# Kernel tuning notes

Hardware: AMD Instinct MI355X
Metric: run time of the kernel (lower is better)

## Reference

```python
import jax, jax.numpy as jnp
import numpy as np

EPS = 1e-12

def sage_layer(x, src, dst, Wl, Wr, b, n_nodes):
    # mean aggregation of source-node features into destination nodes
    msgs = x[src]                                            # [E, F] gather
    s = jax.ops.segment_sum(msgs, dst, num_segments=n_nodes)  # [N, F]
    cnt = jax.ops.segment_sum(jnp.ones((src.shape[0],), x.dtype), dst, num_segments=n_nodes)
    agg = s / jnp.maximum(cnt, 1.0)[:, None]                 # mean; 0 for isolated nodes
    out = agg @ Wl + b + x @ Wr                              # lin_l(agg) + lin_r(x_i)
    norm = jnp.linalg.norm(out, axis=-1, keepdims=True)      # normalize=True -> L2 norm
    return out / jnp.maximum(norm, EPS)


def setup_inputs() -> dict:
    key = jax.random.key(0)
    ks = jax.random.split(key, 8)
    N, E, F = 100000, 1200000, 64
    H1, H2, OUT = 64, 32, 10  # hidden_channels//2, hidden_channels//4, output_dim
    x = jax.random.normal(ks[0], (N, F), dtype=jnp.float32)
    edge_index = jax.random.randint(ks[1], (2, E), 0, N, dtype=jnp.int64)
    def glorot(k, fin, fout):
        lim = np.sqrt(6.0 / (fin + fout)).astype(np.float32)
        return jax.random.uniform(k, (fin, fout), jnp.float32, -lim, lim)
    return {
        "x": x,
        "edge_index": edge_index,
        "W1l": glorot(ks[2], F, H1), "W1r": glorot(ks[3], F, H1), "b1": jnp.zeros((H1,), jnp.float32),
        "W2l": glorot(ks[4], H1, H2), "W2r": glorot(ks[5], H1, H2), "b2": jnp.zeros((H2,), jnp.float32),
        "W3l": glorot(ks[6], H2, OUT), "W3r": glorot(ks[7], H2, OUT), "b3": jnp.zeros((OUT,), jnp.float32),
    }


def reference(x, edge_index, W1l, W1r, b1, W2l, W2r, b2, W3l, W3r, b3):
    n = x.shape[0]
    src, dst = edge_index[0], edge_index[1]
    h = jax.nn.relu(sage_layer(x, src, dst, W1l, W1r, b1, n))
    h = jax.nn.relu(sage_layer(h, src, dst, W2l, W2r, b2, n))
    h = sage_layer(h, src, dst, W3l, W3r, b3, n)
    return jax.nn.log_softmax(h, axis=1)
```

## Files before the change

### kernel.cpp

```cpp
#include <hip/hip_runtime.h>
#include <math.h>


typedef __attribute__((ext_vector_type(8))) short short8;
typedef __attribute__((ext_vector_type(4))) float floatx4;
typedef __attribute__((ext_vector_type(2))) float floatx2;

__device__ __forceinline__ unsigned short f2bf(float f) {
    unsigned u = __float_as_uint(f);
    u += 0x7fffu + ((u >> 16) & 1u);
    return (unsigned short)(u >> 16);
}
__device__ __forceinline__ float blo(unsigned u) { return __uint_as_float(u << 16); }
__device__ __forceinline__ float bhi(unsigned u) { return __uint_as_float(u & 0xffff0000u); }
__device__ __forceinline__ unsigned char f2fp8(float f) {
    return (unsigned char)(__builtin_amdgcn_cvt_pk_fp8_f32(f, f, 0, false) & 0xFF);
}


__global__ __launch_bounds__(256) void hist_kernel(
        const int* __restrict__ ei, int* __restrict__ bh, int* __restrict__ sync_ctr,
        int E, int NB, int NBKT) {
    __shared__ int lh[256];
    const int tid = threadIdx.x, blk = blockIdx.x;
    if (blk == 0 && tid == 0) *sync_ctr = 0;
    lh[tid] = 0;
    __syncthreads();
    const int base = blk << 12;
#pragma unroll
    for (int i = 0; i < 16; ++i) {
        const int e = base + (i << 8) + tid;
        if (e < E) atomicAdd(&lh[min((int)(((unsigned)ei[E + e]) >> 9), NBKT - 1)], 1);
    }
    __syncthreads();
    if (tid < NBKT) bh[tid * NB + blk] = lh[tid];
}

__global__ __launch_bounds__(256) void bscan_kernel(
        const int* __restrict__ bh, int* __restrict__ offs, int* __restrict__ btot,
        int* __restrict__ bucket_base, int* __restrict__ sync_ctr,
        int NB, int NBKT) {
    const int lane = threadIdx.x & 63;
    const int w = blockIdx.x * 4 + (threadIdx.x >> 6);
    if (w < NBKT) {
        int running = 0;
        for (int base = 0; base < NB; base += 64) {
            const int j = base + lane;
            const int v = (j < NB) ? bh[w * NB + j] : 0;
            int incl = v;
#pragma unroll
            for (int off = 1; off < 64; off <<= 1) {
                const int t = __shfl_up(incl, off);
                if (lane >= off) incl += t;
            }
            if (j < NB) offs[w * NB + j] = running + incl - v;
            running += __shfl(incl, 63);
        }
        if (lane == 0) btot[w] = running;
    }
    __threadfence();
    __syncthreads();
    __shared__ int amLast;
    if (threadIdx.x == 0) amLast = (atomicAdd(sync_ctr, 1) == (int)gridDim.x - 1);
    __syncthreads();
    if (amLast && threadIdx.x < 64) {
        __threadfence();
        int running = 0;
        for (int base = 0; base < NBKT; base += 64) {
            const int j = base + threadIdx.x;
            const int v = (j < NBKT) ? btot[j] : 0;
            int incl = v;
#pragma unroll
            for (int off = 1; off < 64; off <<= 1) {
                const int t = __shfl_up(incl, off);
                if ((int)threadIdx.x >= off) incl += t;
            }
            if (j < NBKT) bucket_base[j] = running + incl - v;
            running += __shfl(incl, 63);
        }
        if (threadIdx.x == 0) bucket_base[NBKT] = running;
    }
}

__global__ __launch_bounds__(256) void scatter_kernel(
        const int* __restrict__ ei, const int* __restrict__ offs,
        const int* __restrict__ bucket_base, unsigned* __restrict__ ebuf,
        int E, int NB, int NBKT) {
    __shared__ int lcur[256];
    const int tid = threadIdx.x, blk = blockIdx.x;
    if (tid < NBKT) lcur[tid] = bucket_base[tid] + offs[tid * NB + blk];
    __syncthreads();
    const int base = blk << 12;
#pragma unroll
    for (int i = 0; i < 16; ++i) {
        const int e = base + (i << 8) + tid;
        if (e < E) {
            const int s = ei[e];
            const unsigned d = (unsigned)ei[E + e];
            int p = atomicAdd(&lcur[min((int)(d >> 9), NBKT - 1)], 1);
            p = min(p, E - 1);
            ebuf[p] = ((d & 511u) << 17) | (unsigned)s;
        }
    }
}

__global__ __launch_bounds__(512) void bucket_csr_kernel(
        const unsigned* __restrict__ ebuf, const int* __restrict__ bucket_base,
        int* __restrict__ rowptr, int* __restrict__ deg, int* __restrict__ col,
        int N, int E) {
    __shared__ unsigned long long lcnt[512];
    __shared__ int lcur[2048];
    __shared__ int wsum[8];
    const int b = blockIdx.x, tid = threadIdx.x;
    const int q1 = N >> 2, q2 = N >> 1, q3 = (N >> 2) + (N >> 1);
    const int segbase = bucket_base[b];
    const int L = bucket_base[b + 1] - segbase;
    lcnt[tid] = 0ull;
    __syncthreads();
    for (int i = tid; i < L; i += 512) {
        const unsigned p = ebuf[segbase + i];
        const int ln = p >> 17;
        const int s  = (int)(p & 0x1FFFFu);
        const int q  = (s < q2) ? ((s < q1) ? 0 : 1) : ((s < q3) ? 2 : 3);
        atomicAdd(&lcnt[ln], 1ull << (q << 4));
    }
    __syncthreads();
    const unsigned long long cv = lcnt[tid];
    const int f0 = (int)(cv & 0xFFFFu),         f1 = (int)((cv >> 16) & 0xFFFFu);
    const int f2 = (int)((cv >> 32) & 0xFFFFu), f3 = (int)((cv >> 48) & 0xFFFFu);
    const int dnode = f0 + f1 + f2 + f3;
    const int lane = tid & 63, w = tid >> 6;
    int incl = dnode;
#pragma unroll
    for (int off = 1; off < 64; off <<= 1) {
        const int t = __shfl_up(incl, off);
        if (lane >= off) incl += t;
    }
    if (lane == 63) wsum[w] = incl;
    __syncthreads();
    int wbase = 0;
#pragma unroll
    for (int ww = 0; ww < 8; ++ww) if (ww < w) wbase += wsum[ww];
    const int excl = wbase + incl - dnode;
    const int node = (b << 9) + tid;
    if (node < N) { rowptr[node] = segbase + excl; deg[node] = dnode; }
    lcur[tid]        = excl;
    lcur[512 + tid]  = excl + f0;
    lcur[1024 + tid] = excl + f0 + f1;
    lcur[1536 + tid] = excl + f0 + f1 + f2;
    __syncthreads();
    for (int i = tid; i < L; i += 512) {
        const unsigned p = ebuf[segbase + i];
        const int ln = p >> 17;
        const int s  = (int)(p & 0x1FFFFu);
        const int q  = (s < q2) ? ((s < q1) ? 0 : 1) : ((s < q3) ? 2 : 3);
        int pos = atomicAdd(&lcur[(q << 9) + ln], 1);
        pos = min(segbase + pos, E - 1);
        col[pos] = s;
    }
}

template <int K, int F_OUT, int PAD, bool AFP32, bool YL8>
__global__ __launch_bounds__(256) void transform_kernel(
        const void* __restrict__ Ain, const float* __restrict__ Wl,
        const float* __restrict__ Wr, const float* __restrict__ b,
        void* __restrict__ yl, unsigned short* __restrict__ yr, int n) {
    constexpr int KSTEP = K / 32;
    constexpr int NT = PAD / 16;
    const int lane = threadIdx.x & 63;
    const int wid = (blockIdx.x * blockDim.x + threadIdx.x) >> 6;
    const int ntiles = (n + 15) >> 4;
    if (wid >= ntiles) return;
    const int nl = lane & 15, q = lane >> 4;

    short8 Bl[NT][KSTEP], Br[NT][KSTEP];
    float biasv[NT];
#pragma unroll
    for (int t = 0; t < NT; ++t) {
        const int ncol = t * 16 + nl;
        biasv[t] = (ncol < F_OUT) ? b[ncol] : 0.f;
#pragma unroll
        for (int ks = 0; ks < KSTEP; ++ks) {
#pragma unroll
            for (int j = 0; j < 8; ++j) {
                const int k = ks * 32 + q * 8 + j;
                Bl[t][ks][j] = (ncol < F_OUT) ? (short)f2bf(Wl[k * F_OUT + ncol]) : (short)0;
                Br[t][ks][j] = (ncol < F_OUT) ? (short)f2bf(Wr[k * F_OUT + ncol]) : (short)0;
            }
        }
    }

    const int m0 = wid * 16;
    int m = m0 + nl; if (m >= n) m = n - 1;

    short8 a[KSTEP];
#pragma unroll
    for (int ks = 0; ks < KSTEP; ++ks) {
        if (AFP32) {
            const float* p = (const float*)Ain + (size_t)m * K + ks * 32 + q * 8;
#pragma unroll
            for (int j = 0; j < 8; ++j) a[ks][j] = (short)f2bf(p[j]);
        } else {
            union { uint4 u; short8 s; } cvt;
            cvt.u = *(const uint4*)((const unsigned short*)Ain + (size_t)m * K + ks * 32 + q * 8);
            a[ks] = cvt.s;
        }
    }

    floatx4 accl[NT], accr[NT];
#pragma unroll
    for (int t = 0; t < NT; ++t) { accl[t] = {0.f,0.f,0.f,0.f}; accr[t] = {0.f,0.f,0.f,0.f}; }
#pragma unroll
    for (int ks = 0; ks < KSTEP; ++ks) {
#pragma unroll
        for (int t = 0; t < NT; ++t) {
            accl[t] = __builtin_amdgcn_mfma_f32_16x16x32_bf16(a[ks], Bl[t][ks], accl[t], 0, 0, 0);
            accr[t] = __builtin_amdgcn_mfma_f32_16x16x32_bf16(a[ks], Br[t][ks], accr[t], 0, 0, 0);
        }
    }

#pragma unroll
    for (int t = 0; t < NT; ++t) {
        const int ncol = t * 16 + nl;
#pragma unroll
        for (int r = 0; r < 4; ++r) {
            const int node = m0 + q * 4 + r;
            if (node < n) {
                if (YL8)
                    ((unsigned char*)yl)[(size_t)node * PAD + ncol] = f2fp8(accl[t][r]);
                else
                    ((unsigned short*)yl)[(size_t)node * PAD + ncol] = f2bf(accl[t][r]);
                yr[(size_t)node * PAD + ncol] = f2bf(accr[t][r] + biasv[t]);
            }
        }
    }
}

template <int F, int ACT, int PK>
__global__ __launch_bounds__(256) void agg_kernel(
        const void* __restrict__ yl, const unsigned short* __restrict__ yr,
        const int* __restrict__ rowptr, const int* __restrict__ degv,
        const int* __restrict__ col,
        unsigned short* __restrict__ hout, float* __restrict__ fout, int n) {
    constexpr int G = F / 8;
    constexpr int NPW = 64 / G;
    const int lane = threadIdx.x & 63;
    const int wid = (blockIdx.x * blockDim.x + threadIdx.x) >> 6;
    const int g = lane / G, c = lane % G;
    const int node = wid * NPW + g;
    if (node >= n) return;

    const int beg = rowptr[node];
    const int dg  = degv[node];
    const int nmax = n - 1;

    float a0=0.f,a1=0.f,a2=0.f,a3=0.f,a4=0.f,a5=0.f,a6=0.f,a7=0.f;
    int i = 0;
    if (PK == 1) {
        const unsigned char* base = (const unsigned char*)yl + c * 8;
        auto accrow = [&](uint2 t) {
            const floatx2 p0 = __builtin_amdgcn_cvt_pk_f32_fp8((int)t.x, false);
            const floatx2 p1 = __builtin_amdgcn_cvt_pk_f32_fp8((int)t.x, true);
            const floatx2 p2 = __builtin_amdgcn_cvt_pk_f32_fp8((int)t.y, false);
            const floatx2 p3 = __builtin_amdgcn_cvt_pk_f32_fp8((int)t.y, true);
            a0 += p0.x; a1 += p0.y; a2 += p1.x; a3 += p1.y;
            a4 += p2.x; a5 += p2.y; a6 += p3.x; a7 += p3.y;
        };
        if (dg >= 4) {
            int c0 = col[beg], c1 = col[beg+1], c2 = col[beg+2], c3 = col[beg+3];
            for (; i + 8 <= dg; i += 4) {
                const int d0 = col[beg+i+4], d1 = col[beg+i+5];
                const int d2 = col[beg+i+6], d3 = col[beg+i+7];
                const uint2 t0 = *(const uint2*)(base + (size_t)min(c0,nmax) * F);
                const uint2 t1 = *(const uint2*)(base + (size_t)min(c1,nmax) * F);
                const uint2 t2 = *(const uint2*)(base + (size_t)min(c2,nmax) * F);
                const uint2 t3 = *(const uint2*)(base + (size_t)min(c3,nmax) * F);
                accrow(t0); accrow(t1); accrow(t2); accrow(t3);
                c0 = d0; c1 = d1; c2 = d2; c3 = d3;
            }
            const uint2 t0 = *(const uint2*)(base + (size_t)min(c0,nmax) * F);
            const uint2 t1 = *(const uint2*)(base + (size_t)min(c1,nmax) * F);
            const uint2 t2 = *(const uint2*)(base + (size_t)min(c2,nmax) * F);
            const uint2 t3 = *(const uint2*)(base + (size_t)min(c3,nmax) * F);
            accrow(t0); accrow(t1); accrow(t2); accrow(t3);
            i += 4;
        }
        for (; i < dg; ++i)
            accrow(*(const uint2*)(base + (size_t)min(col[beg+i],nmax) * F));
    } else {
        const unsigned short* base = (const unsigned short*)yl + c * 8;
        auto accrow4 = [&](uint4 t) {
            a0 += blo(t.x); a1 += bhi(t.x); a2 += blo(t.y); a3 += bhi(t.y);
            a4 += blo(t.z); a5 += bhi(t.z); a6 += blo(t.w); a7 += bhi(t.w);
        };
        if (dg >= 4) {
            int c0 = col[beg], c1 = col[beg+1], c2 = col[beg+2], c3 = col[beg+3];
            for (; i + 8 <= dg; i += 4) {
                const int d0 = col[beg+i+4], d1 = col[beg+i+5];
                const int d2 = col[beg+i+6], d3 = col[beg+i+7];
                const uint4 t0 = *(const uint4*)(base + (size_t)min(c0,nmax) * F);
                const uint4 t1 = *(const uint4*)(base + (size_t)min(c1,nmax) * F);
                const uint4 t2 = *(const uint4*)(base + (size_t)min(c2,nmax) * F);
                const uint4 t3 = *(const uint4*)(base + (size_t)min(c3,nmax) * F);
                accrow4(t0); accrow4(t1); accrow4(t2); accrow4(t3);
                c0 = d0; c1 = d1; c2 = d2; c3 = d3;
            }
            const uint4 t0 = *(const uint4*)(base + (size_t)min(c0,nmax) * F);
            const uint4 t1 = *(const uint4*)(base + (size_t)min(c1,nmax) * F);
            const uint4 t2 = *(const uint4*)(base + (size_t)min(c2,nmax) * F);
            const uint4 t3 = *(const uint4*)(base + (size_t)min(c3,nmax) * F);
            accrow4(t0); accrow4(t1); accrow4(t2); accrow4(t3);
            i += 4;
        }
        for (; i < dg; ++i)
            accrow4(*(const uint4*)(base + (size_t)min(col[beg+i],nmax) * F));
    }
    const float inv = (dg > 0) ? 1.f / (float)dg : 0.f;

    const uint4 rv = *(const uint4*)(yr + (size_t)node * F + c * 8);
    float o[8];
    o[0] = a0*inv + blo(rv.x); o[1] = a1*inv + bhi(rv.x);
    o[2] = a2*inv + blo(rv.y); o[3] = a3*inv + bhi(rv.y);
    o[4] = a4*inv + blo(rv.z); o[5] = a5*inv + bhi(rv.z);
    o[6] = a6*inv + blo(rv.w); o[7] = a7*inv + bhi(rv.w);

    float ss = 0.f;
#pragma unroll
    for (int j = 0; j < 8; ++j) ss += o[j] * o[j];
#pragma unroll
    for (int off = 1; off < G; off <<= 1) ss += __shfl_xor(ss, off);
    const float scale = 1.f / fmaxf(sqrtf(ss), 1e-12f);

    if (ACT == 1) {
        uint4 u;
        float h[8];
#pragma unroll
        for (int j = 0; j < 8; ++j) h[j] = fmaxf(o[j] * scale, 0.f);
        u.x = (unsigned)f2bf(h[0]) | ((unsigned)f2bf(h[1]) << 16);
        u.y = (unsigned)f2bf(h[2]) | ((unsigned)f2bf(h[3]) << 16);
        u.z = (unsigned)f2bf(h[4]) | ((unsigned)f2bf(h[5]) << 16);
        u.w = (unsigned)f2bf(h[6]) | ((unsigned)f2bf(h[7]) << 16);
        *(uint4*)(hout + (size_t)node * F + c * 8) = u;
    } else {
#pragma unroll
        for (int j = 0; j < 8; ++j) o[j] *= scale;
        const int cbase = c * 8;
        float m = -INFINITY;
#pragma unroll
        for (int j = 0; j < 8; ++j) if (cbase + j < 10) m = fmaxf(m, o[j]);
        m = fmaxf(m, __shfl_xor(m, 1));
        float s = 0.f;
#pragma unroll
        for (int j = 0; j < 8; ++j) if (cbase + j < 10) s += __expf(o[j] - m);
        s += __shfl_xor(s, 1);
        const float ls = logf(s);
#pragma unroll
        for (int j = 0; j < 8; ++j)
            if (cbase + j < 10) fout[(size_t)node * 10 + cbase + j] = o[j] - m - ls;
    }
}

extern "C" void kernel_launch(void* const* d_in, const int* in_sizes, int n_in,
                              void* d_out, int out_size, void* d_ws, size_t ws_size,
                              hipStream_t stream) {
    const float* x   = (const float*)d_in[0];
    const int*   ei  = (const int*)d_in[1];
    const float* W1l = (const float*)d_in[2];
    const float* W1r = (const float*)d_in[3];
    const float* b1  = (const float*)d_in[4];
    const float* W2l = (const float*)d_in[5];
    const float* W2r = (const float*)d_in[6];
    const float* b2  = (const float*)d_in[7];
    const float* W3l = (const float*)d_in[8];
    const float* W3r = (const float*)d_in[9];
    const float* b3  = (const float*)d_in[10];
    float*       out = (float*)d_out;

    const int N = in_sizes[0] / 64;
    const int E = in_sizes[1] / 2;
    const int NBKT = (N + 511) >> 9;
    const int NB   = (E + 4095) >> 12;

    auto align16 = [](size_t v) { return (v + 15) & ~(size_t)15; };
    char* ws = (char*)d_ws;
    size_t off = 0;
    int* rowptr  = (int*)(ws + off); off = align16(off + (size_t)N * 4);
    int* deg     = (int*)(ws + off); off = align16(off + (size_t)N * 4);
    int* colidx  = (int*)(ws + off); off = align16(off + (size_t)E * 4);
    unsigned* ebuf = (unsigned*)(ws + off); off = align16(off + (size_t)E * 4);
    int* bh      = (int*)(ws + off); off = align16(off + (size_t)NBKT * NB * 4);
    int* offsb   = (int*)(ws + off); off = align16(off + (size_t)NBKT * NB * 4);
    int* btot    = (int*)(ws + off); off = align16(off + (size_t)NBKT * 4);
    int* bbase   = (int*)(ws + off); off = align16(off + (size_t)(NBKT + 1) * 4);
    int* sctr    = (int*)(ws + off); off = align16(off + 16);
    unsigned char*  y1l = (unsigned char*)(ws + off);  off = align16(off + (size_t)N * 64);
    unsigned short* y1r = (unsigned short*)(ws + off); off = align16(off + (size_t)N * 64 * 2);
    unsigned short* h1  = (unsigned short*)(ws + off); off = align16(off + (size_t)N * 64 * 2);
    unsigned char*  y2l = (unsigned char*)(ws + off);  off = align16(off + (size_t)N * 32);
    unsigned short* y2r = (unsigned short*)(ws + off); off = align16(off + (size_t)N * 32 * 2);
    unsigned short* h2  = (unsigned short*)(ws + off); off = align16(off + (size_t)N * 32 * 2);
    unsigned short* y3l = (unsigned short*)(ws + off); off = align16(off + (size_t)N * 16 * 2);
    unsigned short* y3r = (unsigned short*)(ws + off); off = align16(off + (size_t)N * 16 * 2);
    (void)ws_size; (void)n_in; (void)out_size;

    hist_kernel<<<NB, 256, 0, stream>>>(ei, bh, sctr, E, NB, NBKT);
    bscan_kernel<<<(NBKT + 3) / 4, 256, 0, stream>>>(bh, offsb, btot, bbase, sctr, NB, NBKT);
    scatter_kernel<<<NB, 256, 0, stream>>>(ei, offsb, bbase, ebuf, E, NB, NBKT);
    bucket_csr_kernel<<<NBKT, 512, 0, stream>>>(ebuf, bbase, rowptr, deg, colidx, N, E);

    const int ntiles = (N + 15) / 16;
    const int tblocks = (ntiles * 64 + 255) / 256;

    transform_kernel<64, 64, 64, true, true><<<tblocks, 256, 0, stream>>>(
        x, W1l, W1r, b1, y1l, y1r, N);
    agg_kernel<64, 1, 1><<<(N + 31) / 32, 256, 0, stream>>>(
        y1l, y1r, rowptr, deg, colidx, h1, nullptr, N);
    transform_kernel<64, 32, 32, false, true><<<tblocks, 256, 0, stream>>>(
        h1, W2l, W2r, b2, y2l, y2r, N);
    agg_kernel<32, 1, 1><<<(N + 63) / 64, 256, 0, stream>>>(
        y2l, y2r, rowptr, deg, colidx, h2, nullptr, N);
    transform_kernel<32, 10, 16, false, false><<<tblocks, 256, 0, stream>>>(
        h2, W3l, W3r, b3, y3l, y3r, N);
    agg_kernel<16, 2, 0><<<(N + 127) / 128, 256, 0, stream>>>(
        y3l, y3r, rowptr, deg, colidx, nullptr, out, N);
}
```

Measured before the change: 212.3 us.

## Fuse all CSR build and layer kernels into one persistent kernel with grid barriers

Replaces the ten separate launches (histogram, bucket scan, scatter, bucket CSR, three transform and three aggregate kernels) with a single persistent kernel. It is sized from occupancy at 256 CUs and uses a software grid barrier between phases. The layer-1 transform is moved to the front so it runs before the CSR build, and every phase uses grid-stride loops. This removes launch gaps and tail idle time, but adds barrier spin cost and depends on all blocks being co-resident. Grid-stride loops may also give lower occupancy per phase than the tuned per-kernel launches.

```diff
diff --git a/kernel.cpp b/kernel.cpp
--- a/kernel.cpp
+++ b/kernel.cpp
@@ -17,168 +17,63 @@
     return (unsigned char)(__builtin_amdgcn_cvt_pk_fp8_f32(f, f, 0, false) & 0xFF);
 }
 
-
-__global__ __launch_bounds__(256) void hist_kernel(
-        const int* __restrict__ ei, int* __restrict__ bh, int* __restrict__ sync_ctr,
-        int E, int NB, int NBKT) {
-    __shared__ int lh[256];
-    const int tid = threadIdx.x, blk = blockIdx.x;
-    if (blk == 0 && tid == 0) *sync_ctr = 0;
-    lh[tid] = 0;
+__device__ __forceinline__ void grid_barrier(int* cnt, int* gen, int nblk) {
     __syncthreads();
-    const int base = blk << 12;
-#pragma unroll
-    for (int i = 0; i < 16; ++i) {
-        const int e = base + (i << 8) + tid;
-        if (e < E) atomicAdd(&lh[min((int)(((unsigned)ei[E + e]) >> 9), NBKT - 1)], 1);
+    if (threadIdx.x == 0) {
+        __threadfence();
+        const int g = __hip_atomic_load(gen, __ATOMIC_RELAXED, __HIP_MEMORY_SCOPE_AGENT);
+        if (atomicAdd(cnt, 1) == nblk - 1) {
+            __hip_atomic_store(cnt, 0, __ATOMIC_RELAXED, __HIP_MEMORY_SCOPE_AGENT);
+            __hip_atomic_store(gen, g + 1, __ATOMIC_RELEASE, __HIP_MEMORY_SCOPE_AGENT);
+        } else {
+            while (__hip_atomic_load(gen, __ATOMIC_ACQUIRE, __HIP_MEMORY_SCOPE_AGENT) == g)
+                __builtin_amdgcn_s_sleep(1);
+        }
+        __threadfence();
     }
     __syncthreads();
-    if (tid < NBKT) bh[tid * NB + blk] = lh[tid];
-}
-
-__global__ __launch_bounds__(256) void bscan_kernel(
-        const int* __restrict__ bh, int* __restrict__ offs, int* __restrict__ btot,
-        int* __restrict__ bucket_base, int* __restrict__ sync_ctr,
-        int NB, int NBKT) {
-    const int lane = threadIdx.x & 63;
-    const int w = blockIdx.x * 4 + (threadIdx.x >> 6);
-    if (w < NBKT) {
-        int running = 0;
-        for (int base = 0; base < NB; base += 64) {
-            const int j = base + lane;
-            const int v = (j < NB) ? bh[w * NB + j] : 0;
-            int incl = v;
-#pragma unroll
-            for (int off = 1; off < 64; off <<= 1) {
-                const int t = __shfl_up(incl, off);
-                if (lane >= off) incl += t;
-            }
-            if (j < NB) offs[w * NB + j] = running + incl - v;
-            running += __shfl(incl, 63);
-        }
-        if (lane == 0) btot[w] = running;
-    }
-    __threadfence();
+}
+
+__device__ void exscan_to_lds(const int* __restrict__ btot, int nbkt,
+                              int* lbase, int* wscr) {
     __syncthreads();
-    __shared__ int amLast;
-    if (threadIdx.x == 0) amLast = (atomicAdd(sync_ctr, 1) == (int)gridDim.x - 1);
-    __syncthreads();
-    if (amLast && threadIdx.x < 64) {
-        __threadfence();
-        int running = 0;
-        for (int base = 0; base < NBKT; base += 64) {
-            const int j = base + threadIdx.x;
-            const int v = (j < NBKT) ? btot[j] : 0;
-            int incl = v;
-#pragma unroll
-            for (int off = 1; off < 64; off <<= 1) {
-                const int t = __shfl_up(incl, off);
-                if ((int)threadIdx.x >= off) incl += t;
-            }
-            if (j < NBKT) bucket_base[j] = running + incl - v;
-            running += __shfl(incl, 63);
-        }
-        if (threadIdx.x == 0) bucket_base[NBKT] = running;
-    }
-}
-
-__global__ __launch_bounds__(256) void scatter_kernel(
-        const int* __restrict__ ei, const int* __restrict__ offs,
-        const int* __restrict__ bucket_base, unsigned* __restrict__ ebuf,
-        int E, int NB, int NBKT) {
-    __shared__ int lcur[256];
-    const int tid = threadIdx.x, blk = blockIdx.x;
-    if (tid < NBKT) lcur[tid] = bucket_base[tid] + offs[tid * NB + blk];
-    __syncthreads();
-    const int base = blk << 12;
-#pragma unroll
-    for (int i = 0; i < 16; ++i) {
-        const int e = base + (i << 8) + tid;
-        if (e < E) {
-            const int s = ei[e];
-            const unsigned d = (unsigned)ei[E + e];
-            int p = atomicAdd(&lcur[min((int)(d >> 9), NBKT - 1)], 1);
-            p = min(p, E - 1);
-            ebuf[p] = ((d & 511u) << 17) | (unsigned)s;
-        }
-    }
-}
-
-__global__ __launch_bounds__(512) void bucket_csr_kernel(
-        const unsigned* __restrict__ ebuf, const int* __restrict__ bucket_base,
-        int* __restrict__ rowptr, int* __restrict__ deg, int* __restrict__ col,
-        int N, int E) {
-    __shared__ unsigned long long lcnt[512];
-    __shared__ int lcur[2048];
-    __shared__ int wsum[8];
-    const int b = blockIdx.x, tid = threadIdx.x;
-    const int q1 = N >> 2, q2 = N >> 1, q3 = (N >> 2) + (N >> 1);
-    const int segbase = bucket_base[b];
-    const int L = bucket_base[b + 1] - segbase;
-    lcnt[tid] = 0ull;
-    __syncthreads();
-    for (int i = tid; i < L; i += 512) {
-        const unsigned p = ebuf[segbase + i];
-        const int ln = p >> 17;
-        const int s  = (int)(p & 0x1FFFFu);
-        const int q  = (s < q2) ? ((s < q1) ? 0 : 1) : ((s < q3) ? 2 : 3);
-        atomicAdd(&lcnt[ln], 1ull << (q << 4));
-    }
-    __syncthreads();
-    const unsigned long long cv = lcnt[tid];
-    const int f0 = (int)(cv & 0xFFFFu),         f1 = (int)((cv >> 16) & 0xFFFFu);
-    const int f2 = (int)((cv >> 32) & 0xFFFFu), f3 = (int)((cv >> 48) & 0xFFFFu);
-    const int dnode = f0 + f1 + f2 + f3;
+    const int tid = threadIdx.x;
     const int lane = tid & 63, w = tid >> 6;
-    int incl = dnode;
+    const int v = (tid < nbkt) ? btot[tid] : 0;
+    int incl = v;
 #pragma unroll
     for (int off = 1; off < 64; off <<= 1) {
         const int t = __shfl_up(incl, off);
         if (lane >= off) incl += t;
     }
-    if (lane == 63) wsum[w] = incl;
+    if (lane == 63) wscr[w] = incl;
     __syncthreads();
-    int wbase = 0;
-#pragma unroll
-    for (int ww = 0; ww < 8; ++ww) if (ww < w) wbase += wsum[ww];
-    const int excl = wbase + incl - dnode;
-    const int node = (b << 9) + tid;
-    if (node < N) { rowptr[node] = segbase + excl; deg[node] = dnode; }
-    lcur[tid]        = excl;
-    lcur[512 + tid]  = excl + f0;
-    lcur[1024 + tid] = excl + f0 + f1;
-    lcur[1536 + tid] = excl + f0 + f1 + f2;
+    int base = 0;
+#pragma unroll
+    for (int ww = 0; ww < 8; ++ww) if (ww < w) base += wscr[ww];
+    if (tid < nbkt) lbase[tid] = base + incl - v;
+    if (tid == nbkt - 1) lbase[nbkt] = base + incl;
     __syncthreads();
-    for (int i = tid; i < L; i += 512) {
-        const unsigned p = ebuf[segbase + i];
-        const int ln = p >> 17;
-        const int s  = (int)(p & 0x1FFFFu);
-        const int q  = (s < q2) ? ((s < q1) ? 0 : 1) : ((s < q3) ? 2 : 3);
-        int pos = atomicAdd(&lcur[(q << 9) + ln], 1);
-        pos = min(segbase + pos, E - 1);
-        col[pos] = s;
-    }
 }
 
 template <int K, int F_OUT, int PAD, bool AFP32, bool YL8>
-__global__ __launch_bounds__(256) void transform_kernel(
+__device__ void transform_phase(
         const void* __restrict__ Ain, const float* __restrict__ Wl,
-        const float* __restrict__ Wr, const float* __restrict__ b,
-        void* __restrict__ yl, unsigned short* __restrict__ yr, int n) {
+        const float* __restrict__ Wr, const float* __restrict__ bia,
+        void* __restrict__ yl, unsigned short* __restrict__ yr,
+        int n, int wid, int totw) {
     constexpr int KSTEP = K / 32;
     constexpr int NT = PAD / 16;
     const int lane = threadIdx.x & 63;
-    const int wid = (blockIdx.x * blockDim.x + threadIdx.x) >> 6;
+    const int nl = lane & 15, q = lane >> 4;
     const int ntiles = (n + 15) >> 4;
-    if (wid >= ntiles) return;
-    const int nl = lane & 15, q = lane >> 4;
 
     short8 Bl[NT][KSTEP], Br[NT][KSTEP];
     float biasv[NT];
 #pragma unroll
     for (int t = 0; t < NT; ++t) {
         const int ncol = t * 16 + nl;
-        biasv[t] = (ncol < F_OUT) ? b[ncol] : 0.f;
+        biasv[t] = (ncol < F_OUT) ? bia[ncol] : 0.f;
 #pragma unroll
         for (int ks = 0; ks < KSTEP; ++ks) {
 #pragma unroll
@@ -190,174 +85,333 @@
         }
     }
 
-    const int m0 = wid * 16;
-    int m = m0 + nl; if (m >= n) m = n - 1;
-
-    short8 a[KSTEP];
-#pragma unroll
-    for (int ks = 0; ks < KSTEP; ++ks) {
-        if (AFP32) {
-            const float* p = (const float*)Ain + (size_t)m * K + ks * 32 + q * 8;
-#pragma unroll
-            for (int j = 0; j < 8; ++j) a[ks][j] = (short)f2bf(p[j]);
-        } else {
-            union { uint4 u; short8 s; } cvt;
-            cvt.u = *(const uint4*)((const unsigned short*)Ain + (size_t)m * K + ks * 32 + q * 8);
-            a[ks] = cvt.s;
-        }
-    }
-
-    floatx4 accl[NT], accr[NT];
-#pragma unroll
-    for (int t = 0; t < NT; ++t) { accl[t] = {0.f,0.f,0.f,0.f}; accr[t] = {0.f,0.f,0.f,0.f}; }
-#pragma unroll
-    for (int ks = 0; ks < KSTEP; ++ks) {
-#pragma unroll
-        for (int t = 0; t < NT; ++t) {
-            accl[t] = __builtin_amdgcn_mfma_f32_16x16x32_bf16(a[ks], Bl[t][ks], accl[t], 0, 0, 0);
-            accr[t] = __builtin_amdgcn_mfma_f32_16x16x32_bf16(a[ks], Br[t][ks], accr[t], 0, 0, 0);
-        }
-    }
-
-#pragma unroll
-    for (int t = 0; t < NT; ++t) {
-        const int ncol = t * 16 + nl;
-#pragma unroll
-        for (int r = 0; r < 4; ++r) {
-            const int node = m0 + q * 4 + r;
-            if (node < n) {
-                if (YL8)
-                    ((unsigned char*)yl)[(size_t)node * PAD + ncol] = f2fp8(accl[t][r]);
-                else
-                    ((unsigned short*)yl)[(size_t)node * PAD + ncol] = f2bf(accl[t][r]);
-                yr[(size_t)node * PAD + ncol] = f2bf(accr[t][r] + biasv[t]);
+    for (int t = wid; t < ntiles; t += totw) {
+        const int m0 = t * 16;
+        int m = m0 + nl; if (m >= n) m = n - 1;
+
+        short8 a[KSTEP];
+#pragma unroll
+        for (int ks = 0; ks < KSTEP; ++ks) {
+            if (AFP32) {
+                const float* p = (const float*)Ain + (size_t)m * K + ks * 32 + q * 8;
+#pragma unroll
+                for (int j = 0; j < 8; ++j) a[ks][j] = (short)f2bf(p[j]);
+            } else {
+                union { uint4 u; short8 s; } cvt;
+                cvt.u = *(const uint4*)((const unsigned short*)Ain + (size_t)m * K + ks * 32 + q * 8);
+                a[ks] = cvt.s;
+            }
+        }
+
+        floatx4 accl[NT], accr[NT];
+#pragma unroll
+        for (int tt = 0; tt < NT; ++tt) { accl[tt] = {0.f,0.f,0.f,0.f}; accr[tt] = {0.f,0.f,0.f,0.f}; }
+#pragma unroll
+        for (int ks = 0; ks < KSTEP; ++ks) {
+#pragma unroll
+            for (int tt = 0; tt < NT; ++tt) {
+                accl[tt] = __builtin_amdgcn_mfma_f32_16x16x32_bf16(a[ks], Bl[tt][ks], accl[tt], 0, 0, 0);
+                accr[tt] = __builtin_amdgcn_mfma_f32_16x16x32_bf16(a[ks], Br[tt][ks], accr[tt], 0, 0, 0);
+            }
+        }
+
+#pragma unroll
+        for (int tt = 0; tt < NT; ++tt) {
+            const int ncol = tt * 16 + nl;
+#pragma unroll
+            for (int r = 0; r < 4; ++r) {
+                const int node = m0 + q * 4 + r;
+                if (node < n) {
+                    if (YL8)
+                        ((unsigned char*)yl)[(size_t)node * PAD + ncol] = f2fp8(accl[tt][r]);
+                    else
+                        ((unsigned short*)yl)[(size_t)node * PAD + ncol] = f2bf(accl[tt][r]);
+                    yr[(size_t)node * PAD + ncol] = f2bf(accr[tt][r] + biasv[tt]);
+                }
             }
         }
     }
 }
 
 template <int F, int ACT, int PK>
-__global__ __launch_bounds__(256) void agg_kernel(
+__device__ void agg_phase(
         const void* __restrict__ yl, const unsigned short* __restrict__ yr,
         const int* __restrict__ rowptr, const int* __restrict__ degv,
         const int* __restrict__ col,
-        unsigned short* __restrict__ hout, float* __restrict__ fout, int n) {
+        unsigned short* __restrict__ hout, float* __restrict__ fout,
+        int n, int wid, int totw) {
     constexpr int G = F / 8;
     constexpr int NPW = 64 / G;
     const int lane = threadIdx.x & 63;
-    const int wid = (blockIdx.x * blockDim.x + threadIdx.x) >> 6;
     const int g = lane / G, c = lane % G;
-    const int node = wid * NPW + g;
-    if (node >= n) return;
-
-    const int beg = rowptr[node];
-    const int dg  = degv[node];
-    const int nmax = n - 1;
-
-    float a0=0.f,a1=0.f,a2=0.f,a3=0.f,a4=0.f,a5=0.f,a6=0.f,a7=0.f;
-    int i = 0;
-    if (PK == 1) {
-        const unsigned char* base = (const unsigned char*)yl + c * 8;
-        auto accrow = [&](uint2 t) {
-            const floatx2 p0 = __builtin_amdgcn_cvt_pk_f32_fp8((int)t.x, false);
-            const floatx2 p1 = __builtin_amdgcn_cvt_pk_f32_fp8((int)t.x, true);
-            const floatx2 p2 = __builtin_amdgcn_cvt_pk_f32_fp8((int)t.y, false);
-            const floatx2 p3 = __builtin_amdgcn_cvt_pk_f32_fp8((int)t.y, true);
-            a0 += p0.x; a1 += p0.y; a2 += p1.x; a3 += p1.y;
-            a4 += p2.x; a5 += p2.y; a6 += p3.x; a7 += p3.y;
-        };
-        if (dg >= 4) {
-            int c0 = col[beg], c1 = col[beg+1], c2 = col[beg+2], c3 = col[beg+3];
-            for (; i + 8 <= dg; i += 4) {
-                const int d0 = col[beg+i+4], d1 = col[beg+i+5];
-                const int d2 = col[beg+i+6], d3 = col[beg+i+7];
+    const int nw = (n + NPW - 1) / NPW;
+
+    for (int w = wid; w < nw; w += totw) {
+        const int node = w * NPW + g;
+        if (node >= n) continue;
+
+        const int beg = rowptr[node];
+        const int dg  = degv[node];
+        const int nmax = n - 1;
+
+        float a0=0.f,a1=0.f,a2=0.f,a3=0.f,a4=0.f,a5=0.f,a6=0.f,a7=0.f;
+        int i = 0;
+        if (PK == 1) {
+            const unsigned char* base = (const unsigned char*)yl + c * 8;
+            auto accrow = [&](uint2 t) {
+                const floatx2 p0 = __builtin_amdgcn_cvt_pk_f32_fp8((int)t.x, false);
+                const floatx2 p1 = __builtin_amdgcn_cvt_pk_f32_fp8((int)t.x, true);
+                const floatx2 p2 = __builtin_amdgcn_cvt_pk_f32_fp8((int)t.y, false);
+                const floatx2 p3 = __builtin_amdgcn_cvt_pk_f32_fp8((int)t.y, true);
+                a0 += p0.x; a1 += p0.y; a2 += p1.x; a3 += p1.y;
+                a4 += p2.x; a5 += p2.y; a6 += p3.x; a7 += p3.y;
+            };
+            if (dg >= 4) {
+                int c0 = col[beg], c1 = col[beg+1], c2 = col[beg+2], c3 = col[beg+3];
+                for (; i + 8 <= dg; i += 4) {
+                    const int d0 = col[beg+i+4], d1 = col[beg+i+5];
+                    const int d2 = col[beg+i+6], d3 = col[beg+i+7];
+                    const uint2 t0 = *(const uint2*)(base + (size_t)min(c0,nmax) * F);
+                    const uint2 t1 = *(const uint2*)(base + (size_t)min(c1,nmax) * F);
+                    const uint2 t2 = *(const uint2*)(base + (size_t)min(c2,nmax) * F);
+                    const uint2 t3 = *(const uint2*)(base + (size_t)min(c3,nmax) * F);
+                    accrow(t0); accrow(t1); accrow(t2); accrow(t3);
+                    c0 = d0; c1 = d1; c2 = d2; c3 = d3;
+                }
                 const uint2 t0 = *(const uint2*)(base + (size_t)min(c0,nmax) * F);
                 const uint2 t1 = *(const uint2*)(base + (size_t)min(c1,nmax) * F);
                 const uint2 t2 = *(const uint2*)(base + (size_t)min(c2,nmax) * F);
                 const uint2 t3 = *(const uint2*)(base + (size_t)min(c3,nmax) * F);
                 accrow(t0); accrow(t1); accrow(t2); accrow(t3);
-                c0 = d0; c1 = d1; c2 = d2; c3 = d3;
-            }
-            const uint2 t0 = *(const uint2*)(base + (size_t)min(c0,nmax) * F);
-            const uint2 t1 = *(const uint2*)(base + (size_t)min(c1,nmax) * F);
-            const uint2 t2 = *(const uint2*)(base + (size_t)min(c2,nmax) * F);
-            const uint2 t3 = *(const uint2*)(base + (size_t)min(c3,nmax) * F);
-            accrow(t0); accrow(t1); accrow(t2); accrow(t3);
-            i += 4;
-        }
-        for (; i < dg; ++i)
-            accrow(*(const uint2*)(base + (size_t)min(col[beg+i],nmax) * F));
-    } else {
-        const unsigned short* base = (const unsigned short*)yl + c * 8;
-        auto accrow4 = [&](uint4 t) {
-            a0 += blo(t.x); a1 += bhi(t.x); a2 += blo(t.y); a3 += bhi(t.y);
-            a4 += blo(t.z); a5 += bhi(t.z); a6 += blo(t.w); a7 += bhi(t.w);
-        };
-        if (dg >= 4) {
-            int c0 = col[beg], c1 = col[beg+1], c2 = col[beg+2], c3 = col[beg+3];
-            for (; i + 8 <= dg; i += 4) {
-                const int d0 = col[beg+i+4], d1 = col[beg+i+5];
-                const int d2 = col[beg+i+6], d3 = col[beg+i+7];
+                i += 4;
+            }
+            for (; i < dg; ++i)
+                accrow(*(const uint2*)(base + (size_t)min(col[beg+i],nmax) * F));
+        } else {
+            const unsigned short* base = (const unsigned short*)yl + c * 8;
+            auto accrow4 = [&](uint4 t) {
+                a0 += blo(t.x); a1 += bhi(t.x); a2 += blo(t.y); a3 += bhi(t.y);
+                a4 += blo(t.z); a5 += bhi(t.z); a6 += blo(t.w); a7 += bhi(t.w);
+            };
+            if (dg >= 4) {
+                int c0 = col[beg], c1 = col[beg+1], c2 = col[beg+2], c3 = col[beg+3];
+                for (; i + 8 <= dg; i += 4) {
+                    const int d0 = col[beg+i+4], d1 = col[beg+i+5];
+                    const int d2 = col[beg+i+6], d3 = col[beg+i+7];
+                    const uint4 t0 = *(const uint4*)(base + (size_t)min(c0,nmax) * F);
+                    const uint4 t1 = *(const uint4*)(base + (size_t)min(c1,nmax) * F);
+                    const uint4 t2 = *(const uint4*)(base + (size_t)min(c2,nmax) * F);
+                    const uint4 t3 = *(const uint4*)(base + (size_t)min(c3,nmax) * F);
+                    accrow4(t0); accrow4(t1); accrow4(t2); accrow4(t3);
+                    c0 = d0; c1 = d1; c2 = d2; c3 = d3;
+                }
                 const uint4 t0 = *(const uint4*)(base + (size_t)min(c0,nmax) * F);
                 const uint4 t1 = *(const uint4*)(base + (size_t)min(c1,nmax) * F);
                 const uint4 t2 = *(const uint4*)(base + (size_t)min(c2,nmax) * F);
                 const uint4 t3 = *(const uint4*)(base + (size_t)min(c3,nmax) * F);
                 accrow4(t0); accrow4(t1); accrow4(t2); accrow4(t3);
-                c0 = d0; c1 = d1; c2 = d2; c3 = d3;
-            }
-            const uint4 t0 = *(const uint4*)(base + (size_t)min(c0,nmax) * F);
-            const uint4 t1 = *(const uint4*)(base + (size_t)min(c1,nmax) * F);
-            const uint4 t2 = *(const uint4*)(base + (size_t)min(c2,nmax) * F);
-            const uint4 t3 = *(const uint4*)(base + (size_t)min(c3,nmax) * F);
-            accrow4(t0); accrow4(t1); accrow4(t2); accrow4(t3);
-            i += 4;
-        }
-        for (; i < dg; ++i)
-            accrow4(*(const uint4*)(base + (size_t)min(col[beg+i],nmax) * F));
-    }
-    const float inv = (dg > 0) ? 1.f / (float)dg : 0.f;
-
-    const uint4 rv = *(const uint4*)(yr + (size_t)node * F + c * 8);
-    float o[8];
-    o[0] = a0*inv + blo(rv.x); o[1] = a1*inv + bhi(rv.x);
-    o[2] = a2*inv + blo(rv.y); o[3] = a3*inv + bhi(rv.y);
-    o[4] = a4*inv + blo(rv.z); o[5] = a5*inv + bhi(rv.z);
-    o[6] = a6*inv + blo(rv.w); o[7] = a7*inv + bhi(rv.w);
-
-    float ss = 0.f;
-#pragma unroll
-    for (int j = 0; j < 8; ++j) ss += o[j] * o[j];
-#pragma unroll
-    for (int off = 1; off < G; off <<= 1) ss += __shfl_xor(ss, off);
-    const float scale = 1.f / fmaxf(sqrtf(ss), 1e-12f);
-
-    if (ACT == 1) {
-        uint4 u;
-        float h[8];
-#pragma unroll
-        for (int j = 0; j < 8; ++j) h[j] = fmaxf(o[j] * scale, 0.f);
-        u.x = (unsigned)f2bf(h[0]) | ((unsigned)f2bf(h[1]) << 16);
-        u.y = (unsigned)f2bf(h[2]) | ((unsigned)f2bf(h[3]) << 16);
-        u.z = (unsigned)f2bf(h[4]) | ((unsigned)f2bf(h[5]) << 16);
-        u.w = (unsigned)f2bf(h[6]) | ((unsigned)f2bf(h[7]) << 16);
-        *(uint4*)(hout + (size_t)node * F + c * 8) = u;
-    } else {
-#pragma unroll
-        for (int j = 0; j < 8; ++j) o[j] *= scale;
-        const int cbase = c * 8;
-        float m = -INFINITY;
-#pragma unroll
-        for (int j = 0; j < 8; ++j) if (cbase + j < 10) m = fmaxf(m, o[j]);
-        m = fmaxf(m, __shfl_xor(m, 1));
-        float s = 0.f;
-#pragma unroll
-        for (int j = 0; j < 8; ++j) if (cbase + j < 10) s += __expf(o[j] - m);
-        s += __shfl_xor(s, 1);
-        const float ls = logf(s);
-#pragma unroll
-        for (int j = 0; j < 8; ++j)
-            if (cbase + j < 10) fout[(size_t)node * 10 + cbase + j] = o[j] - m - ls;
-    }
+                i += 4;
+            }
+            for (; i < dg; ++i)
+                accrow4(*(const uint4*)(base + (size_t)min(col[beg+i],nmax) * F));
+        }
+        const float inv = (dg > 0) ? 1.f / (float)dg : 0.f;
+
+        const uint4 rv = *(const uint4*)(yr + (size_t)node * F + c * 8);
+        float o[8];
+        o[0] = a0*inv + blo(rv.x); o[1] = a1*inv + bhi(rv.x);
+        o[2] = a2*inv + blo(rv.y); o[3] = a3*inv + bhi(rv.y);
+        o[4] = a4*inv + blo(rv.z); o[5] = a5*inv + bhi(rv.z);
+        o[6] = a6*inv + blo(rv.w); o[7] = a7*inv + bhi(rv.w);
+
+        float ss = 0.f;
+#pragma unroll
+        for (int j = 0; j < 8; ++j) ss += o[j] * o[j];
+#pragma unroll
+        for (int off = 1; off < G; off <<= 1) ss += __shfl_xor(ss, off);
+        const float scale = 1.f / fmaxf(sqrtf(ss), 1e-12f);
+
+        if (ACT == 1) {
+            uint4 u;
+            float h[8];
+#pragma unroll
+            for (int j = 0; j < 8; ++j) h[j] = fmaxf(o[j] * scale, 0.f);
+            u.x = (unsigned)f2bf(h[0]) | ((unsigned)f2bf(h[1]) << 16);
+            u.y = (unsigned)f2bf(h[2]) | ((unsigned)f2bf(h[3]) << 16);
+            u.z = (unsigned)f2bf(h[4]) | ((unsigned)f2bf(h[5]) << 16);
+            u.w = (unsigned)f2bf(h[6]) | ((unsigned)f2bf(h[7]) << 16);
+            *(uint4*)(hout + (size_t)node * F + c * 8) = u;
+        } else {
+#pragma unroll
+            for (int j = 0; j < 8; ++j) o[j] *= scale;
+            const int cbase = c * 8;
+            float m = -INFINITY;
+#pragma unroll
+            for (int j = 0; j < 8; ++j) if (cbase + j < 10) m = fmaxf(m, o[j]);
+            m = fmaxf(m, __shfl_xor(m, 1));
+            float s = 0.f;
+#pragma unroll
+            for (int j = 0; j < 8; ++j) if (cbase + j < 10) s += __expf(o[j] - m);
+            s += __shfl_xor(s, 1);
+            const float ls = logf(s);
+#pragma unroll
+            for (int j = 0; j < 8; ++j)
+                if (cbase + j < 10) fout[(size_t)node * 10 + cbase + j] = o[j] - m - ls;
+        }
+    }
+}
+
+#define SMEM_BYTES 13376
+
+__global__ __launch_bounds__(512, 4) void mega_kernel(
+        const float* __restrict__ x, const int* __restrict__ ei,
+        const float* __restrict__ W1l, const float* __restrict__ W1r, const float* __restrict__ b1,
+        const float* __restrict__ W2l, const float* __restrict__ W2r, const float* __restrict__ b2,
+        const float* __restrict__ W3l, const float* __restrict__ W3r, const float* __restrict__ b3,
+        float* __restrict__ out,
+        int* rowptr, int* deg, int* colidx, unsigned* ebuf,
+        int* bh, int* offsb, int* btot, int* barcnt, int* bargen,
+        unsigned char* y1l, unsigned short* y1r, unsigned short* h1,
+        unsigned char* y2l, unsigned short* y2r, unsigned short* h2,
+        unsigned short* y3l, unsigned short* y3r,
+        int N, int E, int NBKT, int NB, int nblk) {
+    __shared__ __align__(16) char smem[SMEM_BYTES];
+    int* lh    = (int*)smem;
+    unsigned long long* lcnt = (unsigned long long*)smem;
+    int* lcur4 = (int*)(smem + 4096);
+    int* lcurS = (int*)smem;
+    int* lbase = (int*)(smem + 12288);
+    int* wscr  = (int*)(smem + 13320);
+
+    const int blk = blockIdx.x, tid = threadIdx.x;
+    const int wid  = (blk * 512 + tid) >> 6;
+    const int totw = nblk * 8;
+
+    transform_phase<64, 64, 64, true, true>(x, W1l, W1r, b1, y1l, y1r, N, wid, totw);
+
+    for (int chunk = blk; chunk < NB; chunk += nblk) {
+        __syncthreads();
+        if (tid < 256) lh[tid] = 0;
+        __syncthreads();
+        const int base = chunk << 12;
+#pragma unroll
+        for (int i = 0; i < 8; ++i) {
+            const int e = base + (i << 9) + tid;
+            if (e < E) atomicAdd(&lh[min((int)(((unsigned)ei[E + e]) >> 9), NBKT - 1)], 1);
+        }
+        __syncthreads();
+        if (tid < NBKT) bh[tid * NB + chunk] = lh[tid];
+    }
+    grid_barrier(barcnt, bargen, nblk);
+
+    {
+        const int lane = tid & 63;
+        for (int w = blk * 8 + (tid >> 6); w < NBKT; w += nblk * 8) {
+            int running = 0;
+            for (int base = 0; base < NB; base += 64) {
+                const int j = base + lane;
+                const int v = (j < NB) ? bh[w * NB + j] : 0;
+                int incl = v;
+#pragma unroll
+                for (int off = 1; off < 64; off <<= 1) {
+                    const int t = __shfl_up(incl, off);
+                    if (lane >= off) incl += t;
+                }
+                if (j < NB) offsb[w * NB + j] = running + incl - v;
+                running += __shfl(incl, 63);
+            }
+            if (lane == 0) btot[w] = running;
+        }
+    }
+    grid_barrier(barcnt, bargen, nblk);
+
+    exscan_to_lds(btot, NBKT, lbase, wscr);
+    for (int chunk = blk; chunk < NB; chunk += nblk) {
+        __syncthreads();
+        if (tid < NBKT) lcurS[tid] = lbase[tid] + offsb[tid * NB + chunk];
+        __syncthreads();
+        const int base = chunk << 12;
+#pragma unroll
+        for (int i = 0; i < 8; ++i) {
+            const int e = base + (i << 9) + tid;
+            if (e < E) {
+                const int s = ei[e];
+                const unsigned d = (unsigned)ei[E + e];
+                int p = atomicAdd(&lcurS[min((int)(d >> 9), NBKT - 1)], 1);
+                p = min(p, E - 1);
+                ebuf[p] = ((d & 511u) << 17) | (unsigned)s;
+            }
+        }
+    }
+    grid_barrier(barcnt, bargen, nblk);
+
+    exscan_to_lds(btot, NBKT, lbase, wscr);
+    {
+        const int q1 = N >> 2, q2 = N >> 1, q3 = (N >> 2) + (N >> 1);
+        const int lane = tid & 63, w = tid >> 6;
+        for (int b = blk; b < NBKT; b += nblk) {
+            const int segbase = lbase[b];
+            const int L = lbase[b + 1] - segbase;
+            __syncthreads();
+            lcnt[tid] = 0ull;
+            __syncthreads();
+            for (int i = tid; i < L; i += 512) {
+                const unsigned p = ebuf[segbase + i];
+                const int ln = p >> 17;
+                const int s  = (int)(p & 0x1FFFFu);
+                const int q  = (s < q2) ? ((s < q1) ? 0 : 1) : ((s < q3) ? 2 : 3);
+                atomicAdd(&lcnt[ln], 1ull << (q << 4));
+            }
+            __syncthreads();
+            const unsigned long long cv = lcnt[tid];
+            const int f0 = (int)(cv & 0xFFFFu),         f1 = (int)((cv >> 16) & 0xFFFFu);
+            const int f2 = (int)((cv >> 32) & 0xFFFFu), f3 = (int)((cv >> 48) & 0xFFFFu);
+            const int dnode = f0 + f1 + f2 + f3;
+            int incl = dnode;
+#pragma unroll
+            for (int off = 1; off < 64; off <<= 1) {
+                const int t = __shfl_up(incl, off);
+                if (lane >= off) incl += t;
+            }
+            if (lane == 63) wscr[w] = incl;
+            __syncthreads();
+            int wbase = 0;
+#pragma unroll
+            for (int ww = 0; ww < 8; ++ww) if (ww < w) wbase += wscr[ww];
+            const int excl = wbase + incl - dnode;
+            const int node = (b << 9) + tid;
+            if (node < N) { rowptr[node] = segbase + excl; deg[node] = dnode; }
+            lcur4[tid]        = excl;
+            lcur4[512 + tid]  = excl + f0;
+            lcur4[1024 + tid] = excl + f0 + f1;
+            lcur4[1536 + tid] = excl + f0 + f1 + f2;
+            __syncthreads();
+            for (int i = tid; i < L; i += 512) {
+                const unsigned p = ebuf[segbase + i];
+                const int ln = p >> 17;
+                const int s  = (int)(p & 0x1FFFFu);
+                const int q  = (s < q2) ? ((s < q1) ? 0 : 1) : ((s < q3) ? 2 : 3);
+                int pos = atomicAdd(&lcur4[(q << 9) + ln], 1);
+                pos = min(segbase + pos, E - 1);
+                colidx[pos] = s;
+            }
+        }
+    }
+    grid_barrier(barcnt, bargen, nblk);
+
+    agg_phase<64, 1, 1>(y1l, y1r, rowptr, deg, colidx, h1, nullptr, N, wid, totw);
+    grid_barrier(barcnt, bargen, nblk);
+
+    transform_phase<64, 32, 32, false, true>(h1, W2l, W2r, b2, y2l, y2r, N, wid, totw);
+    grid_barrier(barcnt, bargen, nblk);
+
+    agg_phase<32, 1, 1>(y2l, y2r, rowptr, deg, colidx, h2, nullptr, N, wid, totw);
+    grid_barrier(barcnt, bargen, nblk);
+
+    transform_phase<32, 10, 16, false, false>(h2, W3l, W3r, b3, y3l, y3r, N, wid, totw);
+    grid_barrier(barcnt, bargen, nblk);
+
+    agg_phase<16, 2, 0>(y3l, y3r, rowptr, deg, colidx, nullptr, out, N, wid, totw);
 }
 
 extern "C" void kernel_launch(void* const* d_in, const int* in_sizes, int n_in,
@@ -391,8 +445,7 @@
     int* bh      = (int*)(ws + off); off = align16(off + (size_t)NBKT * NB * 4);
     int* offsb   = (int*)(ws + off); off = align16(off + (size_t)NBKT * NB * 4);
     int* btot    = (int*)(ws + off); off = align16(off + (size_t)NBKT * 4);
-    int* bbase   = (int*)(ws + off); off = align16(off + (size_t)(NBKT + 1) * 4);
-    int* sctr    = (int*)(ws + off); off = align16(off + 16);
+    int* barmem  = (int*)(ws + off); off = align16(off + 16);
     unsigned char*  y1l = (unsigned char*)(ws + off);  off = align16(off + (size_t)N * 64);
     unsigned short* y1r = (unsigned short*)(ws + off); off = align16(off + (size_t)N * 64 * 2);
     unsigned short* h1  = (unsigned short*)(ws + off); off = align16(off + (size_t)N * 64 * 2);
@@ -403,24 +456,20 @@
     unsigned short* y3r = (unsigned short*)(ws + off); off = align16(off + (size_t)N * 16 * 2);
     (void)ws_size; (void)n_in; (void)out_size;
 
-    hist_kernel<<<NB, 256, 0, stream>>>(ei, bh, sctr, E, NB, NBKT);
-    bscan_kernel<<<(NBKT + 3) / 4, 256, 0, stream>>>(bh, offsb, btot, bbase, sctr, NB, NBKT);
-    scatter_kernel<<<NB, 256, 0, stream>>>(ei, offsb, bbase, ebuf, E, NB, NBKT);
-    bucket_csr_kernel<<<NBKT, 512, 0, stream>>>(ebuf, bbase, rowptr, deg, colidx, N, E);
-
-    const int ntiles = (N + 15) / 16;
-    const int tblocks = (ntiles * 64 + 255) / 256;
-
-    transform_kernel<64, 64, 64, true, true><<<tblocks, 256, 0, stream>>>(
-        x, W1l, W1r, b1, y1l, y1r, N);
-    agg_kernel<64, 1, 1><<<(N + 31) / 32, 256, 0, stream>>>(
-        y1l, y1r, rowptr, deg, colidx, h1, nullptr, N);
-    transform_kernel<64, 32, 32, false, true><<<tblocks, 256, 0, stream>>>(
-        h1, W2l, W2r, b2, y2l, y2r, N);
-    agg_kernel<32, 1, 1><<<(N + 63) / 64, 256, 0, stream>>>(
-        y2l, y2r, rowptr, deg, colidx, h2, nullptr, N);
-    transform_kernel<32, 10, 16, false, false><<<tblocks, 256, 0, stream>>>(
-        h2, W3l, W3r, b3, y3l, y3r, N);
-    agg_kernel<16, 2, 0><<<(N + 127) / 128, 256, 0, stream>>>(
-        y3l, y3r, rowptr, deg, colidx, nullptr, out, N);
-}
+    static int nblk_cached = 0;
+    if (nblk_cached == 0) {
+        int bpc = 0;
+        if (hipOccupancyMaxActiveBlocksPerMultiprocessor(&bpc, mega_kernel, 512, 0)
+                != hipSuccess || bpc < 1) bpc = 1;
+        if (bpc > 4) bpc = 4;
+        nblk_cached = bpc * 256;
+    }
+    const int nblk = nblk_cached;
+
+    hipMemsetAsync(barmem, 0, 8, stream);
+    mega_kernel<<<nblk, 512, 0, stream>>>(
+        x, ei, W1l, W1r, b1, W2l, W2r, b2, W3l, W3r, b3, out,
+        rowptr, deg, colidx, ebuf, bh, offsb, btot, barmem, barmem + 1,
+        y1l, y1r, h1, y2l, y2r, h2, y3l, y3r,
+        N, E, NBKT, NB, nblk);
+}
```

Result: slower. 595.4 us (+180.5%).

## Merge layer-1 transform into scatter kernel launch to run concurrently

Applied to the files above, without the earlier changes.

The layer-1 dense transform (x @ Wl, x @ Wr via MFMA) is folded into the edge-scatter kernel as extra blocks, so the two independent stages share one launch and can run at the same time on the GPU. This removes one kernel launch and lets the compute-heavy transform fill CUs left idle by the memory-bound scatter. The risk is that block scheduling does not interleave them well, and register pressure from the transform path may limit occupancy of the scatter blocks.

```diff
diff --git a/kernel.cpp b/kernel.cpp
--- a/kernel.cpp
+++ b/kernel.cpp
@@ -82,24 +82,101 @@
     }
 }
 
-__global__ __launch_bounds__(256) void scatter_kernel(
+template <int K, int F_OUT, int PAD, bool AFP32, bool YL8>
+__global__ __launch_bounds__(256) void scatter_t1_kernel(
         const int* __restrict__ ei, const int* __restrict__ offs,
         const int* __restrict__ bucket_base, unsigned* __restrict__ ebuf,
-        int E, int NB, int NBKT) {
+        int E, int NB, int NBKT,
+        const void* __restrict__ Ain, const float* __restrict__ Wl,
+        const float* __restrict__ Wr, const float* __restrict__ b,
+        void* __restrict__ yl, unsigned short* __restrict__ yr, int n) {
     __shared__ int lcur[256];
-    const int tid = threadIdx.x, blk = blockIdx.x;
-    if (tid < NBKT) lcur[tid] = bucket_base[tid] + offs[tid * NB + blk];
-    __syncthreads();
-    const int base = blk << 12;
-#pragma unroll
-    for (int i = 0; i < 16; ++i) {
-        const int e = base + (i << 8) + tid;
-        if (e < E) {
-            const int s = ei[e];
-            const unsigned d = (unsigned)ei[E + e];
-            int p = atomicAdd(&lcur[min((int)(d >> 9), NBKT - 1)], 1);
-            p = min(p, E - 1);
-            ebuf[p] = ((d & 511u) << 17) | (unsigned)s;
+    const int tid = threadIdx.x;
+    if ((int)blockIdx.x < NB) {
+        const int blk = blockIdx.x;
+        if (tid < NBKT) lcur[tid] = bucket_base[tid] + offs[tid * NB + blk];
+        __syncthreads();
+        const int base = blk << 12;
+#pragma unroll
+        for (int i = 0; i < 16; ++i) {
+            const int e = base + (i << 8) + tid;
+            if (e < E) {
+                const int s = ei[e];
+                const unsigned d = (unsigned)ei[E + e];
+                int p = atomicAdd(&lcur[min((int)(d >> 9), NBKT - 1)], 1);
+                p = min(p, E - 1);
+                ebuf[p] = ((d & 511u) << 17) | (unsigned)s;
+            }
+        }
+        return;
+    }
+    constexpr int KSTEP = K / 32;
+    constexpr int NT = PAD / 16;
+    const int lane = tid & 63;
+    const int wid = (((int)blockIdx.x - NB) * 256 + tid) >> 6;
+    const int ntiles = (n + 15) >> 4;
+    if (wid >= ntiles) return;
+    const int nl = lane & 15, q = lane >> 4;
+
+    short8 Bl[NT][KSTEP], Br[NT][KSTEP];
+    float biasv[NT];
+#pragma unroll
+    for (int t = 0; t < NT; ++t) {
+        const int ncol = t * 16 + nl;
+        biasv[t] = (ncol < F_OUT) ? b[ncol] : 0.f;
+#pragma unroll
+        for (int ks = 0; ks < KSTEP; ++ks) {
+#pragma unroll
+            for (int j = 0; j < 8; ++j) {
+                const int k = ks * 32 + q * 8 + j;
+                Bl[t][ks][j] = (ncol < F_OUT) ? (short)f2bf(Wl[k * F_OUT + ncol]) : (short)0;
+                Br[t][ks][j] = (ncol < F_OUT) ? (short)f2bf(Wr[k * F_OUT + ncol]) : (short)0;
+            }
+        }
+    }
+
+    const int m0 = wid * 16;
+    int m = m0 + nl; if (m >= n) m = n - 1;
+
+    short8 a[KSTEP];
+#pragma unroll
+    for (int ks = 0; ks < KSTEP; ++ks) {
+        if (AFP32) {
+            const float* p = (const float*)Ain + (size_t)m * K + ks * 32 + q * 8;
+#pragma unroll
+            for (int j = 0; j < 8; ++j) a[ks][j] = (short)f2bf(p[j]);
+        } else {
+            union { uint4 u; short8 s; } cvt;
+            cvt.u = *(const uint4*)((const unsigned short*)Ain + (size_t)m * K + ks * 32 + q * 8);
+            a[ks] = cvt.s;
+        }
+    }
+
+    floatx4 accl[NT], accr[NT];
+#pragma unroll
+    for (int t = 0; t < NT; ++t) { accl[t] = {0.f,0.f,0.f,0.f}; accr[t] = {0.f,0.f,0.f,0.f}; }
+#pragma unroll
+    for (int ks = 0; ks < KSTEP; ++ks) {
+#pragma unroll
+        for (int t = 0; t < NT; ++t) {
+            accl[t] = __builtin_amdgcn_mfma_f32_16x16x32_bf16(a[ks], Bl[t][ks], accl[t], 0, 0, 0);
+            accr[t] = __builtin_amdgcn_mfma_f32_16x16x32_bf16(a[ks], Br[t][ks], accr[t], 0, 0, 0);
+        }
+    }
+
+#pragma unroll
+    for (int t = 0; t < NT; ++t) {
+        const int ncol = t * 16 + nl;
+#pragma unroll
+        for (int r = 0; r < 4; ++r) {
+            const int node = m0 + q * 4 + r;
+            if (node < n) {
+                if (YL8)
+                    ((unsigned char*)yl)[(size_t)node * PAD + ncol] = f2fp8(accl[t][r]);
+                else
+                    ((unsigned short*)yl)[(size_t)node * PAD + ncol] = f2bf(accl[t][r]);
+                yr[(size_t)node * PAD + ncol] = f2bf(accr[t][r] + biasv[t]);
+            }
         }
     }
 }
@@ -403,16 +480,16 @@
     unsigned short* y3r = (unsigned short*)(ws + off); off = align16(off + (size_t)N * 16 * 2);
     (void)ws_size; (void)n_in; (void)out_size;
 
+    const int ntiles = (N + 15) / 16;
+    const int tblocks = (ntiles * 64 + 255) / 256;
+
     hist_kernel<<<NB, 256, 0, stream>>>(ei, bh, sctr, E, NB, NBKT);
     bscan_kernel<<<(NBKT + 3) / 4, 256, 0, stream>>>(bh, offsb, btot, bbase, sctr, NB, NBKT);
-    scatter_kernel<<<NB, 256, 0, stream>>>(ei, offsb, bbase, ebuf, E, NB, NBKT);
+    scatter_t1_kernel<64, 64, 64, true, true><<<NB + tblocks, 256, 0, stream>>>(
+        ei, offsb, bbase, ebuf, E, NB, NBKT,
+        x, W1l, W1r, b1, y1l, y1r, N);
     bucket_csr_kernel<<<NBKT, 512, 0, stream>>>(ebuf, bbase, rowptr, deg, colidx, N, E);
 
-    const int ntiles = (N + 15) / 16;
-    const int tblocks = (ntiles * 64 + 255) / 256;
-
-    transform_kernel<64, 64, 64, true, true><<<tblocks, 256, 0, stream>>>(
-        x, W1l, W1r, b1, y1l, y1r, N);
     agg_kernel<64, 1, 1><<<(N + 31) / 32, 256, 0, stream>>>(
         y1l, y1r, rowptr, deg, colidx, h1, nullptr, N);
     transform_kernel<64, 32, 32, false, true><<<tblocks, 256, 0, stream>>>(
```

New measurement: 206.7 us. 2.6% less time.
